# Performance work log

Hardware: AMD Instinct MI355X
Metric: run time of the kernel (lower is better)

Reference implementation:

```python
import jax, jax.numpy as jnp
import numpy as np

D = 128      # n_hidden
NC = 4       # n_chan
DEPTH = 2
VD_DEPTH = 1
VD_ATTACH = 0
NV = 100000  # n_verts
PE_LEVELS = 6


def _mlp(x, Ws, bs):
    # MLP: Linear -> ReLU -> Linear -> ReLU -> Linear
    h = jax.nn.relu(x @ Ws[0] + bs[0])
    h = jax.nn.relu(h @ Ws[1] + bs[1])
    return h @ Ws[2] + bs[2]


def setup_inputs() -> dict:
    key = jax.random.key(0)
    ks = jax.random.split(key, 20)
    N, H, W = 2, 512, 512
    inp = {}
    inp["vert_idx_img"] = jax.random.randint(ks[0], (N, H, W, 3), 0, NV, dtype=jnp.int64) if jax.config.read("jax_enable_x64") else jax.random.randint(ks[0], (N, H, W, 3), 0, NV, dtype=jnp.int32)
    inp["bary_img"] = jax.random.uniform(ks[1], (N, H, W, 3), dtype=jnp.float32)
    inp["view_dir"] = jax.random.normal(ks[2], (N, H, W, 3), dtype=jnp.float32)
    # params
    s = D ** (-0.5)
    inp["emb_table"] = jax.random.normal(ks[3], (NV + 1, D), dtype=jnp.float32) * s
    k_lin = np.sqrt(2.0 / D).astype(np.float32)
    inp["vde_W"] = jax.random.normal(ks[4], (3 * PE_LEVELS, D), dtype=jnp.float32) * np.sqrt(2.0 / (3 * PE_LEVELS)).astype(np.float32)
    inp["vde_b"] = jnp.zeros((D,), jnp.float32)
    inp["vh_W"] = jax.random.normal(ks[5], (VD_DEPTH, 3, D, D), dtype=jnp.float32) * k_lin
    inp["vh_b"] = jnp.zeros((VD_DEPTH, 3, D), jnp.float32)
    inp["hid_W"] = jax.random.normal(ks[6], (DEPTH, 3, D, D), dtype=jnp.float32) * k_lin
    inp["hid_b"] = jnp.zeros((DEPTH, 3, D), jnp.float32)
    inp["head_W0"] = jax.random.normal(ks[7], (D, D), dtype=jnp.float32) * k_lin
    inp["head_b0"] = jnp.zeros((D,), jnp.float32)
    inp["head_W1"] = jax.random.normal(ks[8], (D, D), dtype=jnp.float32) * k_lin
    inp["head_b1"] = jnp.zeros((D,), jnp.float32)
    inp["head_W2"] = jax.random.normal(ks[9], (D, NC), dtype=jnp.float32) * k_lin
    inp["head_b2"] = jnp.zeros((NC,), jnp.float32)
    return inp


def reference(vert_idx_img, bary_img, view_dir, emb_table, vde_W, vde_b, vh_W, vh_b,
              hid_W, hid_b, head_W0, head_b0, head_W1, head_b1, head_W2, head_b2):
    # --- embedding gather with max_norm=1.0 renorm (torch nn.Embedding semantics)
    idx = vert_idx_img + 1                       # [N,H,W,3]
    e = emb_table[idx]                           # [N,H,W,3,D]
    nrm = jnp.linalg.norm(e, axis=-1, keepdims=True)
    e = e * jnp.where(nrm > 1.0, 1.0 / (nrm + 1e-7), 1.0)
    # --- barycentric weighted sum over the 3 face vertices
    v = jnp.sum(e * bary_img[..., None], axis=3)  # [N,H,W,D]
    # --- view-direction sin/cos positional encoding (proj_dims=6, val=0.9)
    ll = PE_LEVELS // 2
    exb = 2.0 * jnp.arange(ll, dtype=jnp.float32) / PE_LEVELS
    sigma = 2.0 * jnp.pi / jnp.power(0.9, exb)    # [3]
    pe = view_dir[..., None] * sigma              # [N,H,W,3,3]
    pe = jnp.concatenate([jnp.sin(pe), jnp.cos(pe)], axis=-1)  # [N,H,W,3,6]
    pe = pe.reshape(pe.shape[:-2] + (3 * PE_LEVELS,))           # [N,H,W,18]
    vh = pe @ vde_W + vde_b                       # [N,H,W,D]
    for i in range(vh_W.shape[0]):
        vh = jax.nn.relu(_mlp(vh, vh_W[i], vh_b[i]))
    # --- hidden MLP chain with view-dir modulation at viewdirs_attach
    h = v
    for i in range(hid_W.shape[0]):
        h = jax.nn.relu(_mlp(h, hid_W[i], hid_b[i]))
        if i == VD_ATTACH:
            h = h * vh
    # --- head MLP -> rgba
    rgb = _mlp(h, (head_W0, head_W1, head_W2), (head_b0, head_b1, head_b2))
    return rgb
```

## Files before the change

kernel.cpp:

```cpp
#include <hip/hip_runtime.h>

typedef unsigned int  u32;
typedef unsigned short u16;
typedef __attribute__((ext_vector_type(8))) _Float16 h8;
typedef __attribute__((ext_vector_type(2))) _Float16 h2;
typedef __attribute__((ext_vector_type(4))) float    f4;

#define RS    136
#define PRS   40
#define PIXB  128
#define WOFF  5120
#define WT    16384
#define MFMA16 __builtin_amdgcn_mfma_f32_16x16x32_f16

__device__ __forceinline__ u16 f2h(float f) {
  _Float16 h = (_Float16)f;
  return __builtin_bit_cast(u16, h);
}
__device__ __forceinline__ u32 pkrtz(float a, float b) {
  return __builtin_bit_cast(u32, __builtin_amdgcn_cvt_pkrtz(a, b));
}
__device__ __forceinline__ u32 pkmul(u32 a, u32 b) {
  h2 r = __builtin_bit_cast(h2, a) * __builtin_bit_cast(h2, b);
  return __builtin_bit_cast(u32, r);
}
__device__ __forceinline__ u32 pkmax0(u32 a) {
  h2 z = {(_Float16)0.f, (_Float16)0.f};
  h2 r = __builtin_elementwise_max(__builtin_bit_cast(h2, a), z);
  return __builtin_bit_cast(u32, r);
}

__global__ __launch_bounds__(256) void rc_prep(
    const float* __restrict__ vde_W, const float* __restrict__ vh_W,
    const float* __restrict__ hid_W, const float* __restrict__ head_W0,
    const float* __restrict__ head_W1, const float* __restrict__ head_W2,
    u16* __restrict__ ws)
{
  const int TOT = WOFF + 12 * WT;
  int i = blockIdx.x * 256 + threadIdx.x;
  if (i >= TOT) return;
  float val = 0.f;
  if (i < WOFF) {
    int n = i / PRS, k = i - n * PRS;
    if (k < 18) val = vde_W[k * 128 + n];
  } else {
    int t = i - WOFF;
    int j = t >> 14;
    int rr = t & 16383;
    int n = rr >> 7, kq = rr & 127;
    int k = kq ^ ((n & 7) << 3);
    if (j < 3)        val = vh_W[j * 16384 + k * 128 + n];
    else if (j < 9)   val = hid_W[(j - 3) * 16384 + k * 128 + n];
    else if (j == 9)  val = head_W0[k * 128 + n];
    else if (j == 10) val = head_W1[k * 128 + n];
    else              val = (n < 4) ? head_W2[k * 4 + n] : 0.f;
  }
  ws[i] = f2h(val);
}

#define STAGE(j) do {                                                         \
  const u16* _s = ws + WOFF + (j) * WT + w * 512 + lane * 8;                  \
  _Pragma("unroll")                                                           \
  for (int _it = 0; _it < 4; ++_it)                                           \
    __builtin_amdgcn_global_load_lds(                                         \
        (const __attribute__((address_space(1))) void*)(_s + _it * 4096),     \
        (__attribute__((address_space(3))) void*)&WL[w * 512 + _it * 4096],   \
        16, 0, 0);                                                            \
} while (0)

#define LOADA(AA, NTL) do {                                                   \
  _Pragma("unroll")                                                           \
  for (int ks = 0; ks < 4; ++ks)                                              \
    AA[ks] = *(const h8*)&WL[(nbase + (NTL) * 16 + r) * 128 +                 \
                             ((ks * 32 + g * 8) ^ rsw)];                      \
} while (0)

#define COMPUTE_NT(NTL, AA) do {                                              \
  f4 bini = *(const f4*)&BL[blb + nbase + (NTL) * 16 + 4 * g];                \
  f4 ac[2] = {bini, bini};                                                    \
  _Pragma("unroll")                                                           \
  for (int ks = 0; ks < 4; ++ks) {                                            \
    ac[0] = MFMA16(AA[ks], x[0][ks], ac[0], 0, 0, 0);                         \
    ac[1] = MFMA16(AA[ks], x[1][ks], ac[1], 0, 0, 0);                         \
  }                                                                           \
  const int col = nbase + (NTL) * 16 + 4 * g;                                 \
  _Pragma("unroll")                                                           \
  for (int t = 0; t < 2; ++t) {                                               \
    u32 lo = pkmax0(pkrtz(ac[t][0], ac[t][1]));                               \
    u32 hi = pkmax0(pkrtz(ac[t][2], ac[t][3]));                               \
    if (mode == 1) {                                 \
      vhp[t][NTL][0] = lo; vhp[t][NTL][1] = hi;                               \
    } else {                                                                  \
      if (mode == 2) {                                \
        lo = pkmul(lo, vhp[t][NTL][0]);                                       \
        hi = pkmul(hi, vhp[t][NTL][1]);                                       \
      }                                                                       \
      *(uint2*)&X[xr[t] + col] = make_uint2(lo, hi);                          \
    }                                                                         \
  }                                                                           \
} while (0)

#define LAYER(LI) do {                                                        \
  const int li   = (LI);                                                      \
  const int blb  = (li + 1) * 128;                                            \
  const int mode = (li == 2) ? 1 : (li == 5) ? 2 : 0;                         \
  h8 x[2][4];                                                                 \
  _Pragma("unroll")                                                           \
  for (int t = 0; t < 2; ++t)                                                 \
    _Pragma("unroll")                                                         \
    for (int ks = 0; ks < 4; ++ks)                                            \
      x[t][ks] = *(const h8*)&X[xr[t] + ks * 32 + g * 8];                     \
  h8 Aa[4], Ab[4];                                                            \
  LOADA(Aa, 0); LOADA(Ab, 1);                                                 \
  __syncthreads();                   \
  COMPUTE_NT(0, Aa);  LOADA(Aa, 2);                                           \
  COMPUTE_NT(1, Ab);  LOADA(Ab, 3);                                           \
  COMPUTE_NT(2, Aa);                                                          \
  COMPUTE_NT(3, Ab);                                                          \
  if (li == 2) { __syncthreads(); do_gather(); }                              \
  __syncthreads();                          \
  STAGE(li + 1);                                                              \
  __syncthreads();                     \
} while (0)

__global__ __launch_bounds__(512, 4) void rc_main(
    const int*   __restrict__ vert,  const float* __restrict__ bary,
    const float* __restrict__ view,  const float* __restrict__ emb,
    const float* __restrict__ vde_b, const float* __restrict__ vh_b,
    const float* __restrict__ hid_b, const float* __restrict__ head_b0,
    const float* __restrict__ head_b1, const float* __restrict__ head_b2,
    const u16*   __restrict__ ws,    float* __restrict__ out)
{
  __shared__ __align__(16) u16   X[PIXB * RS];
  __shared__ __align__(16) u16   WL[WT];
  __shared__ __align__(16) float BL[1664];

  const int tid  = threadIdx.x;
  const int lane = tid & 63;
  const int w    = tid >> 6;
  const int pg   = w >> 1;
  const int cg   = w & 1;
  const int r    = lane & 15;
  const int g    = lane >> 4;
  const int pbase = pg * 32;
  const int nbase = cg * 64;
  const int rsw  = (r & 7) << 3;
  const size_t bpix = (size_t)blockIdx.x * PIXB;

  for (int i = tid; i < 1664; i += 512) {
    float v;
    if      (i < 128)  v = vde_b[i];
    else if (i < 512)  v = vh_b[i - 128];
    else if (i < 1280) v = hid_b[i - 512];
    else if (i < 1408) v = head_b0[i - 1280];
    else if (i < 1536) v = head_b1[i - 1408];
    else if (i < 1540) v = head_b2[i - 1536];
    else               v = 0.f;
    BL[i] = v;
  }

  if (tid < PIXB) {
    const int p = tid;
    const float* vd = view + (bpix + p) * 3;
    const float SG0 = 6.28318530718f;
    const float SG1 = 6.50777324f;
    const float SG2 = 6.74038866f;
    u32 pw[16];
#pragma unroll
    for (int i = 0; i < 3; ++i) {
      float x = vd[i];
      float s0 = __sinf(x * SG0), c0 = __cosf(x * SG0);
      float s1 = __sinf(x * SG1), c1 = __cosf(x * SG1);
      float s2 = __sinf(x * SG2), c2 = __cosf(x * SG2);
      pw[i * 3 + 0] = (u32)f2h(s0) | ((u32)f2h(s1) << 16);
      pw[i * 3 + 1] = (u32)f2h(s2) | ((u32)f2h(c0) << 16);
      pw[i * 3 + 2] = (u32)f2h(c1) | ((u32)f2h(c2) << 16);
    }
#pragma unroll
    for (int q = 9; q < 16; ++q) pw[q] = 0u;
    uint4* dst = (uint4*)&X[p * RS];
#pragma unroll
    for (int q = 0; q < 4; ++q)
      dst[q] = make_uint4(pw[4*q], pw[4*q+1], pw[4*q+2], pw[4*q+3]);
  }
  __syncthreads();

  const int xr[2] = { (pbase + r) * RS, (pbase + 16 + r) * RS };

  auto do_gather = [&]() {
#pragma unroll 4
    for (int i = 0; i < 4; ++i) {
      int p = w * 16 + g * 4 + i;
      size_t gp = bpix + p;
      const int*   vi = vert + gp * 3;
      const float* by = bary + gp * 3;
      f4 va = {0.f,0.f,0.f,0.f}, vb = {0.f,0.f,0.f,0.f};
#pragma unroll
      for (int vt = 0; vt < 3; ++vt) {
        int id = vi[vt] + 1;
        const float* row = emb + (size_t)id * 128 + r * 8;
        f4 e0 = *(const f4*)row;
        f4 e1 = *(const f4*)(row + 4);
        float ss = e0[0]*e0[0] + e0[1]*e0[1] + e0[2]*e0[2] + e0[3]*e0[3]
                 + e1[0]*e1[0] + e1[1]*e1[1] + e1[2]*e1[2] + e1[3]*e1[3];
        ss += __shfl_xor(ss, 1);
        ss += __shfl_xor(ss, 2);
        ss += __shfl_xor(ss, 4);
        ss += __shfl_xor(ss, 8);
        float nrm = sqrtf(ss);
        float sc  = (nrm > 1.f) ? (1.f / (nrm + 1e-7f)) : 1.f;
        float wt  = by[vt] * sc;
#pragma unroll
        for (int j = 0; j < 4; ++j) { va[j] += wt * e0[j]; vb[j] += wt * e1[j]; }
      }
      h8 o;
#pragma unroll
      for (int j = 0; j < 4; ++j) { o[j] = (_Float16)va[j]; o[j+4] = (_Float16)vb[j]; }
      *(h8*)&X[p * RS + r * 8] = o;
    }
  };

  STAGE(0);
  {
    h8 Av[4];
#pragma unroll
    for (int ntl = 0; ntl < 4; ++ntl)
      Av[ntl] = *(const h8*)&ws[(nbase + ntl * 16 + r) * PRS + g * 8];
    h8 pe[2];
#pragma unroll
    for (int t = 0; t < 2; ++t) pe[t] = *(const h8*)&X[xr[t] + g * 8];
    __syncthreads();
#pragma unroll
    for (int ntl = 0; ntl < 4; ++ntl) {
      f4 bini = *(const f4*)&BL[nbase + ntl * 16 + 4 * g];
      const int col = nbase + ntl * 16 + 4 * g;
#pragma unroll
      for (int t = 0; t < 2; ++t) {
        f4 acc = MFMA16(Av[ntl], pe[t], bini, 0, 0, 0);
        *(uint2*)&X[xr[t] + col] =
          make_uint2(pkrtz(acc[0], acc[1]), pkrtz(acc[2], acc[3]));
      }
    }
  }
  __syncthreads();

  u32 vhp[2][4][2];
  LAYER(0);  LAYER(1);  LAYER(2);  LAYER(3);
  LAYER(4);  LAYER(5);  LAYER(6);  LAYER(7);
  LAYER(8);  LAYER(9);  LAYER(10);

  if (cg == 0) {
    h8 x[2][4];
#pragma unroll
    for (int t = 0; t < 2; ++t)
#pragma unroll
      for (int ks = 0; ks < 4; ++ks)
        x[t][ks] = *(const h8*)&X[xr[t] + ks * 32 + g * 8];
    f4 b2 = *(const f4*)&BL[1536 + 4 * g];
    f4 acc[2] = {b2, b2};
#pragma unroll
    for (int ks = 0; ks < 4; ++ks) {
      h8 A = *(const h8*)&WL[r * 128 + ((ks * 32 + g * 8) ^ rsw)];
#pragma unroll
      for (int t = 0; t < 2; ++t)
        acc[t] = MFMA16(A, x[t][ks], acc[t], 0, 0, 0);
    }
    if (g == 0) {
#pragma unroll
      for (int t = 0; t < 2; ++t)
        *(f4*)&out[(bpix + pbase + t * 16 + r) * 4] = acc[t];
    }
  }
}

extern "C" void kernel_launch(void* const* d_in, const int* in_sizes, int n_in,
                              void* d_out, int out_size, void* d_ws, size_t ws_size,
                              hipStream_t stream) {
  const int*   vert    = (const int*)  d_in[0];
  const float* bary    = (const float*)d_in[1];
  const float* view    = (const float*)d_in[2];
  const float* emb     = (const float*)d_in[3];
  const float* vde_W   = (const float*)d_in[4];
  const float* vde_b   = (const float*)d_in[5];
  const float* vh_W    = (const float*)d_in[6];
  const float* vh_b    = (const float*)d_in[7];
  const float* hid_W   = (const float*)d_in[8];
  const float* hid_b   = (const float*)d_in[9];
  const float* head_W0 = (const float*)d_in[10];
  const float* head_b0 = (const float*)d_in[11];
  const float* head_W1 = (const float*)d_in[12];
  const float* head_b1 = (const float*)d_in[13];
  const float* head_W2 = (const float*)d_in[14];
  const float* head_b2 = (const float*)d_in[15];
  u16* wsp = (u16*)d_ws;

  rc_prep<<<788, 256, 0, stream>>>(vde_W, vh_W, hid_W, head_W0, head_W1, head_W2, wsp);
  rc_main<<<4096, 512, 0, stream>>>(vert, bary, view, emb, vde_b, vh_b, hid_b,
                                    head_b0, head_b1, head_b2, wsp, (float*)d_out);
}
```

Before: 348.6 us.

## Stream MLP weights directly from global into registers, dropping LDS weight staging

Repacks weights in the prep kernel into an MFMA-fragment-major layout so each lane can load its A operands with contiguous dwordx4 global loads. The main kernel stops staging each layer's weight tile into LDS: it issues inline-asm global loads into register triple-buffers and gates each compute step with explicit vmcnt waits. This removes the 32KB LDS weight buffer and the extra barriers around staging, which may allow more blocks per CU. The cost is that every wave now re-reads the weights from L2/global each layer, and correctness depends on hand-counted vmcnt values.

```diff
diff --git a/kernel.cpp b/kernel.cpp
--- a/kernel.cpp
+++ b/kernel.cpp
@@ -1,6 +1,7 @@
 #include <hip/hip_runtime.h>
 
 typedef unsigned int  u32;
+typedef unsigned long long u64;
 typedef unsigned short u16;
 typedef __attribute__((ext_vector_type(8))) _Float16 h8;
 typedef __attribute__((ext_vector_type(2))) _Float16 h2;
@@ -10,7 +11,7 @@
 #define PRS   40
 #define PIXB  128
 #define WOFF  5120
-#define WT    16384
+#define FULLT 16384
 #define MFMA16 __builtin_amdgcn_mfma_f32_16x16x32_f16
 
 __device__ __forceinline__ u16 f2h(float f) {
@@ -36,7 +37,7 @@
     const float* __restrict__ head_W1, const float* __restrict__ head_W2,
     u16* __restrict__ ws)
 {
-  const int TOT = WOFF + 12 * WT;
+  const int TOT = WOFF + 12 * FULLT;
   int i = blockIdx.x * 256 + threadIdx.x;
   if (i >= TOT) return;
   float val = 0.f;
@@ -44,11 +45,16 @@
     int n = i / PRS, k = i - n * PRS;
     if (k < 18) val = vde_W[k * 128 + n];
   } else {
-    int t = i - WOFF;
-    int j = t >> 14;
-    int rr = t & 16383;
-    int n = rr >> 7, kq = rr & 127;
-    int k = kq ^ ((n & 7) << 3);
+    int t  = i - WOFF;
+    int j  = t >> 14;
+    int c  = t & 16383;
+    int nt = c >> 11;
+    int ks = (c >> 9) & 3;
+    int ln = (c >> 3) & 63;
+    int e  = c & 7;
+    int r  = ln & 15, g = ln >> 4;
+    int n  = nt * 16 + r;
+    int k  = ks * 32 + g * 8 + e;
     if (j < 3)        val = vh_W[j * 16384 + k * 128 + n];
     else if (j < 9)   val = hid_W[(j - 3) * 16384 + k * 128 + n];
     else if (j == 9)  val = head_W0[k * 128 + n];
@@ -58,21 +64,21 @@
   ws[i] = f2h(val);
 }
 
-#define STAGE(j) do {                                                         \
-  const u16* _s = ws + WOFF + (j) * WT + w * 512 + lane * 8;                  \
-  _Pragma("unroll")                                                           \
-  for (int _it = 0; _it < 4; ++_it)                                           \
-    __builtin_amdgcn_global_load_lds(                                         \
-        (const __attribute__((address_space(1))) void*)(_s + _it * 4096),     \
-        (__attribute__((address_space(3))) void*)&WL[w * 512 + _it * 4096],   \
-        16, 0, 0);                                                            \
+#define GLOAD(dst, base, voff, immstr)                                        \
+  asm volatile("global_load_dwordx4 %0, %1, %2 offset:" immstr               \
+               : "=v"(dst) : "v"(voff), "s"(base) : "memory")
+
+#define ISSUE(S, NTL) do {                                                    \
+  u32 vo_ = aoff + (NTL) * 4096;                                              \
+  GLOAD(Ar##S[0], wbase, vo_, "0");                                           \
+  GLOAD(Ar##S[1], wbase, vo_, "1024");                                        \
+  GLOAD(Ar##S[2], wbase, vo_, "2048");                                        \
+  GLOAD(Ar##S[3], wbase, vo_, "3072");                                        \
 } while (0)
 
-#define LOADA(AA, NTL) do {                                                   \
-  _Pragma("unroll")                                                           \
-  for (int ks = 0; ks < 4; ++ks)                                              \
-    AA[ks] = *(const h8*)&WL[(nbase + (NTL) * 16 + r) * 128 +                 \
-                             ((ks * 32 + g * 8) ^ rsw)];                      \
+#define WAITV(nstr) do {                                                      \
+  asm volatile("s_waitcnt vmcnt(" nstr ")" ::: "memory");                     \
+  __builtin_amdgcn_sched_barrier(0);                                          \
 } while (0)
 
 #define COMPUTE_NT(NTL, AA) do {                                              \
@@ -104,23 +110,21 @@
   const int li   = (LI);                                                      \
   const int blb  = (li + 1) * 128;                                            \
   const int mode = (li == 2) ? 1 : (li == 5) ? 2 : 0;                         \
+  const u64 wbase = (u64)(uintptr_t)(ws + WOFF + li * FULLT);                 \
+  ISSUE(0, 0); ISSUE(1, 1); ISSUE(2, 2);              \
   h8 x[2][4];                                                                 \
   _Pragma("unroll")                                                           \
   for (int t = 0; t < 2; ++t)                                                 \
     _Pragma("unroll")                                                         \
     for (int ks = 0; ks < 4; ++ks)                                            \
       x[t][ks] = *(const h8*)&X[xr[t] + ks * 32 + g * 8];                     \
-  h8 Aa[4], Ab[4];                                                            \
-  LOADA(Aa, 0); LOADA(Ab, 1);                                                 \
-  __syncthreads();                   \
-  COMPUTE_NT(0, Aa);  LOADA(Aa, 2);                                           \
-  COMPUTE_NT(1, Ab);  LOADA(Ab, 3);                                           \
-  COMPUTE_NT(2, Aa);                                                          \
-  COMPUTE_NT(3, Ab);                                                          \
+  __syncthreads();                  \
+  WAITV("8");  COMPUTE_NT(0, Ar0);  ISSUE(0, 3);                              \
+  WAITV("8");  COMPUTE_NT(1, Ar1);                                            \
+  WAITV("4");  COMPUTE_NT(2, Ar2);                                            \
+  WAITV("0");  COMPUTE_NT(3, Ar0);                                            \
   if (li == 2) { __syncthreads(); do_gather(); }                              \
-  __syncthreads();                          \
-  STAGE(li + 1);                                                              \
-  __syncthreads();                     \
+  __syncthreads();                                      \
 } while (0)
 
 __global__ __launch_bounds__(512, 4) void rc_main(
@@ -132,7 +136,6 @@
     const u16*   __restrict__ ws,    float* __restrict__ out)
 {
   __shared__ __align__(16) u16   X[PIXB * RS];
-  __shared__ __align__(16) u16   WL[WT];
   __shared__ __align__(16) float BL[1664];
 
   const int tid  = threadIdx.x;
@@ -144,7 +147,7 @@
   const int g    = lane >> 4;
   const int pbase = pg * 32;
   const int nbase = cg * 64;
-  const int rsw  = (r & 7) << 3;
+  const u32 aoff  = (u32)(cg * 16384 + lane * 16);
   const size_t bpix = (size_t)blockIdx.x * PIXB;
 
   for (int i = tid; i < 1664; i += 512) {
@@ -220,7 +223,6 @@
     }
   };
 
-  STAGE(0);
   {
     h8 Av[4];
 #pragma unroll
@@ -245,6 +247,7 @@
   __syncthreads();
 
   u32 vhp[2][4][2];
+  h8 Ar0[4], Ar1[4], Ar2[4];
   LAYER(0);  LAYER(1);  LAYER(2);  LAYER(3);
   LAYER(4);  LAYER(5);  LAYER(6);  LAYER(7);
   LAYER(8);  LAYER(9);  LAYER(10);
@@ -256,11 +259,12 @@
 #pragma unroll
       for (int ks = 0; ks < 4; ++ks)
         x[t][ks] = *(const h8*)&X[xr[t] + ks * 32 + g * 8];
+    const u16* wa = ws + WOFF + 11 * FULLT;
     f4 b2 = *(const f4*)&BL[1536 + 4 * g];
     f4 acc[2] = {b2, b2};
 #pragma unroll
     for (int ks = 0; ks < 4; ++ks) {
-      h8 A = *(const h8*)&WL[r * 128 + ((ks * 32 + g * 8) ^ rsw)];
+      h8 A = *(const h8*)&wa[ks * 512 + lane * 8];
 #pragma unroll
       for (int t = 0; t < 2; ++t)
         acc[t] = MFMA16(A, x[t][ks], acc[t], 0, 0, 0);
```

Measured after the change: 313.3 us. 1.11x faster.
